# Kernel optimization log

Measured on AMD Instinct MI355X. Metric: run time of the kernel, lower is better.

The kernel has to match this reference:

```python
import jax, jax.numpy as jnp
import numpy as np

B, T = 64, 512
V, E, H, L = 100000, 256, 256, 9


def _lstm(x, Wx, Wh, b):
    # x: [B,T,E] -> hs: [B,T,H]; Keras gate order i,f,c,o
    xg = jnp.einsum('bte,eg->btg', x, Wx) + b  # [B,T,4H]
    h0 = jnp.zeros((x.shape[0], Wh.shape[0]), x.dtype)

    def step(carry, xt):
        h, c = carry
        g = xt + h @ Wh
        i, f, gc, o = jnp.split(g, 4, axis=-1)
        c = jax.nn.sigmoid(f) * c + jax.nn.sigmoid(i) * jnp.tanh(gc)
        h = jax.nn.sigmoid(o) * jnp.tanh(c)
        return (h, c), h

    _, hs = jax.lax.scan(step, (h0, h0), jnp.swapaxes(xg, 0, 1))
    return jnp.swapaxes(hs, 0, 1)


def _crf_log_likelihood(logits, tags, seq_len, trans):
    # logits: [B,T,L], tags: [B,T] int, seq_len: [B] int, trans: [L,L]
    Bb, Tt, Ll = logits.shape
    t_idx = jnp.arange(Tt)
    mask = (t_idx[None, :] < seq_len[:, None]).astype(logits.dtype)  # [B,T]
    # gold path score: unary + pairwise transitions
    unary = jnp.take_along_axis(logits, tags[..., None], axis=-1)[..., 0]  # [B,T]
    unary_score = jnp.sum(unary * mask, axis=-1)
    binary = trans[tags[:, :-1], tags[:, 1:]]  # [B,T-1]
    binary_score = jnp.sum(binary * mask[:, 1:], axis=-1)
    score = unary_score + binary_score
    # forward algorithm (log partition)
    alpha0 = logits[:, 0]  # [B,L]
    step_mask = t_idx[1:, None] < seq_len[None, :]  # [T-1,B]

    def step(alpha, xs):
        logit_t, m = xs  # [B,L], [B]
        new = jax.nn.logsumexp(alpha[:, :, None] + trans[None], axis=1) + logit_t
        alpha = jnp.where(m[:, None], new, alpha)
        return alpha, None

    alpha, _ = jax.lax.scan(step, alpha0, (jnp.swapaxes(logits[:, 1:], 0, 1), step_mask))
    log_norm = jax.nn.logsumexp(alpha, axis=-1)  # [B]
    return score - log_norm


def setup_inputs() -> dict:
    key = jax.random.key(0)
    ks = jax.random.split(key, 12)
    s = 0.05
    return {
        'tokens': jax.random.randint(ks[0], (B, T), 0, V),
        'labels': jax.random.randint(ks[1], (B, T), 0, L),
        'emb_table': jax.random.normal(ks[2], (V, E), jnp.float32) * s,
        'Wx_f': jax.random.normal(ks[3], (E, 4 * H), jnp.float32) * s,
        'Wh_f': jax.random.normal(ks[4], (H, 4 * H), jnp.float32) * s,
        'b_f': jnp.zeros((4 * H,), jnp.float32),
        'Wx_b': jax.random.normal(ks[5], (E, 4 * H), jnp.float32) * s,
        'Wh_b': jax.random.normal(ks[6], (H, 4 * H), jnp.float32) * s,
        'b_b': jnp.zeros((4 * H,), jnp.float32),
        'W_dense': jax.random.normal(ks[7], (2 * H, L), jnp.float32) * s,
        'b_dense': jnp.zeros((L,), jnp.float32),
        'trans': jax.random.uniform(ks[8], (L, L), jnp.float32),
    }


def reference(tokens, labels, emb_table, Wx_f, Wh_f, b_f, Wx_b, Wh_b, b_b, W_dense, b_dense, trans):
    # seq_len = count of non-pad (nonzero) tokens, as in the original call()
    seq_len = jnp.sum((tokens != 0).astype(jnp.int32), axis=-1)  # [B]
    emb = emb_table[tokens]  # [B,T,E]  (dropout inactive at inference)
    h_fwd = _lstm(emb, Wx_f, Wh_f, b_f)
    h_bwd = _lstm(emb[:, ::-1], Wx_b, Wh_b, b_b)[:, ::-1]
    enc = jnp.concatenate([h_fwd, h_bwd], axis=-1)  # [B,T,2H]
    logits = enc @ W_dense + b_dense  # [B,T,L]
    ll = _crf_log_likelihood(logits, labels, seq_len, trans)  # [B]
    return logits, seq_len, ll
```

## Files before the change

### kernel.cpp

```cpp
#include <hip/hip_runtime.h>
#include <hip/hip_fp16.h>


typedef unsigned int  uint32;
typedef unsigned short ushort16;
typedef __attribute__((ext_vector_type(8))) short  short8;
typedef __attribute__((ext_vector_type(4))) float  floatx4;
typedef __attribute__((ext_vector_type(2))) _Float16 half2t;

#define BB 64
#define TT 512
#define NT (BB*TT)
#define G4 1024
#define NL 9
#define KR 92
#define KL 36

__device__ inline float bf2f(ushort16 u) {
  return __builtin_bit_cast(float, ((uint32)u) << 16);
}
__device__ inline ushort16 f2bf(float f) {
  uint32 u = __builtin_bit_cast(uint32, f);
  u += 0x7fffu + ((u >> 16) & 1u);
  return (ushort16)(u >> 16);
}
__device__ inline float sigf(float x)  { return 1.0f / (1.0f + __expf(-x)); }
__device__ inline float tanhf_(float x){ return 1.0f - 2.0f / (1.0f + __expf(2.0f * x)); }

__device__ inline float fdot2_(uint32 w, half2t h, float acc) {
  return __builtin_amdgcn_fdot2(__builtin_bit_cast(half2t, w), h, acc, false);
}

__global__ __launch_bounds__(64) void k_seqlen(const int* __restrict__ tokens,
                                               int* __restrict__ slen,
                                               float* __restrict__ out_sl) {
  const int b = blockIdx.x, lane = threadIdx.x;
  int cnt = 0;
  for (int t = lane; t < TT; t += 64) cnt += (tokens[b * TT + t] != 0) ? 1 : 0;
  #pragma unroll
  for (int off = 32; off >= 1; off >>= 1) cnt += __shfl_down(cnt, off, 64);
  if (lane == 0) { slen[b] = cnt; out_sl[b] = (float)cnt; }
}

__global__ __launch_bounds__(256) void k_embed(const int* __restrict__ tokens,
                                               const float* __restrict__ emb,
                                               ushort16* __restrict__ A) {
  const int f = blockIdx.x * 256 + threadIdx.x;
  const int e = f * 4;
  const int row = e >> 8;
  const int col = e & 255;
  const int tok = tokens[row];
  const float4 v = *(const float4*)(emb + (size_t)tok * 256 + col);
  uint32 lo = (uint32)f2bf(v.x) | ((uint32)f2bf(v.y) << 16);
  uint32 hi = (uint32)f2bf(v.z) | ((uint32)f2bf(v.w) << 16);
  *(uint2*)(A + e) = make_uint2(lo, hi);
}

__global__ __launch_bounds__(256) void k_wxprep(const float* __restrict__ Wxf,
                                                const float* __restrict__ Wxb,
                                                ushort16* __restrict__ BT) {
  const int id = blockIdx.x * 256 + threadIdx.x;
  const int c = id >> 8, k = id & 255;
  const float v = (c < G4) ? Wxf[k * G4 + c] : Wxb[k * G4 + (c - G4)];
  BT[c * 256 + k] = f2bf(v);
}

__global__ __launch_bounds__(256) void k_whprep(const float* __restrict__ Wh,
                                                uint32* __restrict__ W2) {
  const int id = blockIdx.x * 256 + threadIdx.x;
  const int k2 = id >> 10, c = id & 1023;
  const float w0 = Wh[(2 * k2) * G4 + c];
  const float w1 = Wh[(2 * k2 + 1) * G4 + c];
  const ushort16 b0 = __builtin_bit_cast(ushort16, (_Float16)w0);
  const ushort16 b1 = __builtin_bit_cast(ushort16, (_Float16)w1);
  W2[id] = ((uint32)b1 << 16) | (uint32)b0;
}

__global__ __launch_bounds__(256) void k_gemm_xg(const ushort16* __restrict__ A,
                                                 const ushort16* __restrict__ BT,
                                                 const float* __restrict__ bias_f,
                                                 const float* __restrict__ bias_b,
                                                 ushort16* __restrict__ xgf,
                                                 ushort16* __restrict__ xgb) {
  __shared__ __align__(16) ushort16 As[64 * 36];
  __shared__ __align__(16) ushort16 Bs[64 * 36];
  const int m0 = blockIdx.x * 64;
  const int n0 = blockIdx.y * 64;
  const int tid = threadIdx.x;
  const int wave = tid >> 6, lane = tid & 63;
  const int lr = tid >> 2;
  const int lc = (tid & 3) * 8;
  const int am = lane & 15, aq = lane >> 4;
  floatx4 acc[4];
  #pragma unroll
  for (int j = 0; j < 4; ++j) acc[j] = (floatx4){0.f, 0.f, 0.f, 0.f};

  for (int k0 = 0; k0 < 256; k0 += 32) {
    const uint4 va = *(const uint4*)(A  + ((m0 + lr) * 256 + k0 + lc));
    const uint4 vb = *(const uint4*)(BT + ((n0 + lr) * 256 + k0 + lc));
    *(uint2*)&As[lr * 36 + lc]     = make_uint2(va.x, va.y);
    *(uint2*)&As[lr * 36 + lc + 4] = make_uint2(va.z, va.w);
    *(uint2*)&Bs[lr * 36 + lc]     = make_uint2(vb.x, vb.y);
    *(uint2*)&Bs[lr * 36 + lc + 4] = make_uint2(vb.z, vb.w);
    __syncthreads();
    union { uint2 u[2]; short8 s; } fa, fb;
    fa.u[0] = *(const uint2*)&As[(wave * 16 + am) * 36 + aq * 8];
    fa.u[1] = *(const uint2*)&As[(wave * 16 + am) * 36 + aq * 8 + 4];
    #pragma unroll
    for (int j = 0; j < 4; ++j) {
      fb.u[0] = *(const uint2*)&Bs[(j * 16 + am) * 36 + aq * 8];
      fb.u[1] = *(const uint2*)&Bs[(j * 16 + am) * 36 + aq * 8 + 4];
      acc[j] = __builtin_amdgcn_mfma_f32_16x16x32_bf16(fa.s, fb.s, acc[j], 0, 0, 0);
    }
    __syncthreads();
  }
  const int orow = m0 + wave * 16 + aq * 4;
  #pragma unroll
  for (int j = 0; j < 4; ++j) {
    const int col = n0 + j * 16 + am;
    const float bv = (col < G4) ? bias_f[col] : bias_b[col - G4];
    #pragma unroll
    for (int r = 0; r < 4; ++r) {
      const float v = acc[j][r] + bv;
      const int row = orow + r;
      if (col < G4) xgf[row * G4 + col] = f2bf(v);
      else          xgb[row * G4 + (col - G4)] = f2bf(v);
    }
  }
}

__global__ __launch_bounds__(512, 2) void k_lstm(const ushort16* __restrict__ xgf,
                                                 const ushort16* __restrict__ xgb,
                                                 const uint32* __restrict__ Whf,
                                                 const uint32* __restrict__ Whb,
                                                 float* __restrict__ enc) {
  __shared__ uint32 WL[KL * 1024];
  __shared__ float gate[1024];
  __shared__ __align__(16) uint32 h2buf[2][128];
  const int bi = blockIdx.x;
  const int dir = bi >> 6, b = bi & 63;
  const int tid = threadIdx.x;
  const int w = tid >> 6, l = tid & 63;
  const int colA = w * 128 + l;
  const int colB = colA + 64;
  const ushort16* xg = dir ? xgb : xgf;
  const uint32* W2 = dir ? Whb : Whf;

  for (int idx = tid; idx < KL * 1024; idx += 512) {
    const int k2r = idx >> 10, c = idx & 1023;
    WL[(c >> 7) * (KL * 128) + k2r * 128 + ((c & 63) << 1) + ((c >> 6) & 1)] =
        W2[(KR + k2r) * 1024 + c];
  }
  uint32 wA[KR], wB[KR];
  #pragma unroll
  for (int i = 0; i < KR; ++i) {
    wA[i] = W2[i * 1024 + colA];
    wB[i] = W2[i * 1024 + colB];
  }
  #pragma unroll
  for (int i = 0; i < KR; ++i) asm volatile("" : "+v"(wA[i]), "+v"(wB[i]));

  if (tid < 128) h2buf[0][tid] = 0u;
  float c_state = 0.f;
  __syncthreads();

  const uint32* wl = WL + w * (KL * 128) + (l << 1);
  {
  }
  const int t0 = dir ? (TT - 1) : 0;
  ushort16 xA = xg[(size_t)(b * TT + t0) * G4 + colA];
  ushort16 xB = xg[(size_t)(b * TT + t0) * G4 + colB];

  for (int s = 0; s < TT; ++s) {
    float acc0 = bf2f(xA);
    float acc1 = 0.f;
    float acc2 = bf2f(xB);
    float acc3 = 0.f;
    if (s + 1 < TT) {
      const int t1 = dir ? (TT - 2 - s) : (s + 1);
      const ushort16* xr1 = xg + (size_t)(b * TT + t1) * G4;
      xA = xr1[colA];
      xB = xr1[colB];
    }
    const uint4* hb = (const uint4*)h2buf[s & 1];
    #pragma unroll
    for (int blk = 0; blk < 32; ++blk) {
      const uint4 hq = hb[blk];
      #pragma unroll
      for (int j = 0; j < 4; ++j) {
        const int k2 = blk * 4 + j;
        const uint32 hu = (j == 0) ? hq.x : (j == 1) ? hq.y : (j == 2) ? hq.z : hq.w;
        const half2t hh = __builtin_bit_cast(half2t, hu);
        if (k2 < KR) {
          if (j & 1) { acc1 = fdot2_(wA[k2], hh, acc1); acc3 = fdot2_(wB[k2], hh, acc3); }
          else       { acc0 = fdot2_(wA[k2], hh, acc0); acc2 = fdot2_(wB[k2], hh, acc2); }
        } else {
          const uint2 wp = *(const uint2*)(wl + (k2 - KR) * 128);
          if (j & 1) { acc1 = fdot2_(wp.x, hh, acc1); acc3 = fdot2_(wp.y, hh, acc3); }
          else       { acc0 = fdot2_(wp.x, hh, acc0); acc2 = fdot2_(wp.y, hh, acc2); }
        }
      }
    }
    gate[colA] = acc0 + acc1;
    gate[colB] = acc2 + acc3;
    __syncthreads();
    if (tid < 256) {
      const float gi = gate[tid];
      const float gf = gate[256 + tid];
      const float gg = gate[512 + tid];
      const float go = gate[768 + tid];
      c_state = sigf(gf) * c_state + sigf(gi) * tanhf_(gg);
      const float h = sigf(go) * tanhf_(c_state);
      const int row = b * TT + (dir ? (TT - 1 - s) : s);
      enc[(size_t)row * 512 + dir * 256 + tid] = h;
      const int hv = (int)(uint32)__builtin_bit_cast(ushort16, (_Float16)h);
      const int ho = __shfl_xor(hv, 1, 64);
      if (!(tid & 1))
        h2buf[(s + 1) & 1][tid >> 1] = ((uint32)hv & 0xffffu) | ((uint32)ho << 16);
    }
    __syncthreads();
  }
}

__global__ __launch_bounds__(256) void k_dense(const float* __restrict__ enc,
                                               const float* __restrict__ Wd,
                                               const float* __restrict__ bd,
                                               float* __restrict__ logits) {
  __shared__ float Wl[512 * NL];
  __shared__ float bl[NL];
  const int tid = threadIdx.x;
  for (int i = tid; i < 512 * NL; i += 256) Wl[i] = Wd[i];
  if (tid < NL) bl[tid] = bd[tid];
  __syncthreads();
  const int wave = tid >> 6, lane = tid & 63;
  const int row = blockIdx.x * 4 + wave;
  const float* er = enc + (size_t)row * 512;
  float p[NL];
  #pragma unroll
  for (int c = 0; c < NL; ++c) p[c] = 0.f;
  #pragma unroll
  for (int u = 0; u < 8; ++u) {
    const int k = u * 64 + lane;
    const float v = er[k];
    const float* wr = &Wl[k * NL];
    #pragma unroll
    for (int c = 0; c < NL; ++c) p[c] += v * wr[c];
  }
  #pragma unroll
  for (int c = 0; c < NL; ++c) {
    #pragma unroll
    for (int off = 32; off >= 1; off >>= 1) p[c] += __shfl_down(p[c], off, 64);
  }
  if (lane == 0) {
    float* orow = logits + (size_t)row * NL;
    #pragma unroll
    for (int c = 0; c < NL; ++c) orow[c] = p[c] + bl[c];
  }
}

__global__ __launch_bounds__(64) void k_crf(const float* __restrict__ logits,
                                            const int* __restrict__ labels,
                                            const int* __restrict__ slen,
                                            const float* __restrict__ trans,
                                            float* __restrict__ out_ll) {
  __shared__ float tr[NL * NL];
  __shared__ float alpha[NL];
  const int b = blockIdx.x;
  const int lane = threadIdx.x;
  for (int i = lane; i < NL * NL; i += 64) tr[i] = trans[i];
  __syncthreads();
  const int len = slen[b];
  const int* tg = labels + b * TT;
  const float* lg = logits + (size_t)b * TT * NL;
  float s = 0.f;
  for (int t = lane; t < TT; t += 64)
    if (t < len) s += lg[t * NL + tg[t]];
  for (int t = lane; t < TT - 1; t += 64)
    if (t + 1 < len) s += tr[tg[t] * NL + tg[t + 1]];
  #pragma unroll
  for (int off = 32; off >= 1; off >>= 1) s += __shfl_down(s, off, 64);
  if (lane < NL) alpha[lane] = lg[lane];
  __syncthreads();
  if (lane < NL) {
    const int j = lane;
    for (int t = 1; t < TT; ++t) {
      if (t < len) {
        float av[NL];
        float m = -1e30f;
        #pragma unroll
        for (int i = 0; i < NL; ++i) { av[i] = alpha[i] + tr[i * NL + j]; m = fmaxf(m, av[i]); }
        float ss = 0.f;
        #pragma unroll
        for (int i = 0; i < NL; ++i) ss += __expf(av[i] - m);
        const float nj = m + __logf(ss) + lg[t * NL + j];
        alpha[j] = nj;
      }
    }
  }
  __syncthreads();
  if (lane == 0) {
    float m = -1e30f;
    #pragma unroll
    for (int i = 0; i < NL; ++i) m = fmaxf(m, alpha[i]);
    float ss = 0.f;
    #pragma unroll
    for (int i = 0; i < NL; ++i) ss += __expf(alpha[i] - m);
    out_ll[b] = s - (m + __logf(ss));
  }
}

extern "C" void kernel_launch(void* const* d_in, const int* in_sizes, int n_in,
                              void* d_out, int out_size, void* d_ws, size_t ws_size,
                              hipStream_t stream) {
  (void)in_sizes; (void)n_in; (void)out_size; (void)ws_size;
  const int*   tokens = (const int*)d_in[0];
  const int*   labels = (const int*)d_in[1];
  const float* emb    = (const float*)d_in[2];
  const float* Wxf    = (const float*)d_in[3];
  const float* Whf    = (const float*)d_in[4];
  const float* bf_    = (const float*)d_in[5];
  const float* Wxb    = (const float*)d_in[6];
  const float* Whb    = (const float*)d_in[7];
  const float* bb_    = (const float*)d_in[8];
  const float* Wd     = (const float*)d_in[9];
  const float* bd     = (const float*)d_in[10];
  const float* trans  = (const float*)d_in[11];
  float* out = (float*)d_out;

  char* ws = (char*)d_ws;
  ushort16* A    = (ushort16*)(ws + 0);
  ushort16* BT   = (ushort16*)(ws + 16777216);
  uint32*   W2f  = (uint32*)  (ws + 17825792);
  uint32*   W2b  = (uint32*)  (ws + 18350080);
  ushort16* xgf  = (ushort16*)(ws + 18874368);
  ushort16* xgb  = (ushort16*)(ws + 85983232);
  float*    enc  = (float*)   (ws + 153092096);
  int*      slen = (int*)     (ws + 220200960);

  k_seqlen<<<BB, 64, 0, stream>>>(tokens, slen, out + NT * NL);
  k_embed <<<NT * 256 / 4 / 256, 256, 0, stream>>>(tokens, emb, A);
  k_wxprep<<<2048 * 256 / 256, 256, 0, stream>>>(Wxf, Wxb, BT);
  k_whprep<<<128 * 1024 / 256, 256, 0, stream>>>(Whf, W2f);
  k_whprep<<<128 * 1024 / 256, 256, 0, stream>>>(Whb, W2b);
  k_gemm_xg<<<dim3(NT / 64, 2048 / 64), 256, 0, stream>>>(A, BT, bf_, bb_, xgf, xgb);
  k_lstm  <<<128, 512, 0, stream>>>(xgf, xgb, W2f, W2b, enc);
  k_dense <<<NT / 4, 256, 0, stream>>>(enc, Wd, bd, out);
  k_crf   <<<BB, 64, 0, stream>>>(out, labels, slen, trans, out + NT * NL + BB);
}
```

Before: 1.403 ms.

## Keep LSTM recurrent weights in AGPRs and pack xg gate pairs per thread

The recurrent-weight register arrays in the LSTM kernel now live in accumulator registers (AGPRs), written once with v_accvgpr_write and read back each step with v_accvgpr_read. This frees architectural VGPRs so more weights can stay in registers rather than spill. Separately, the xg GEMM epilogue writes its output in a permuted layout so each LSTM thread fetches its two gate inputs with one 32-bit load instead of two 16-bit loads. The cost is an extra accvgpr read per weight on every timestep of the serial recurrence.

Result: slower. 1.919 ms (+36.8%).

```diff
diff --git a/kernel.cpp b/kernel.cpp
--- a/kernel.cpp
+++ b/kernel.cpp
@@ -119,18 +119,20 @@
   for (int j = 0; j < 4; ++j) {
     const int col = n0 + j * 16 + am;
     const float bv = (col < G4) ? bias_f[col] : bias_b[col - G4];
+    const int cc = col & 1023;
+    const int poff = ((cc >> 7) * 64 + (cc & 63)) * 2 + ((cc >> 6) & 1);
+    ushort16* dst = (col < G4) ? xgf : xgb;
     #pragma unroll
     for (int r = 0; r < 4; ++r) {
       const float v = acc[j][r] + bv;
       const int row = orow + r;
-      if (col < G4) xgf[row * G4 + col] = f2bf(v);
-      else          xgb[row * G4 + (col - G4)] = f2bf(v);
-    }
-  }
-}
-
-__global__ __launch_bounds__(512, 2) void k_lstm(const ushort16* __restrict__ xgf,
-                                                 const ushort16* __restrict__ xgb,
+      dst[(size_t)row * G4 + poff] = f2bf(v);
+    }
+  }
+}
+
+__global__ __launch_bounds__(512, 2) void k_lstm(const uint32* __restrict__ xgf,
+                                                 const uint32* __restrict__ xgb,
                                                  const uint32* __restrict__ Whf,
                                                  const uint32* __restrict__ Whb,
                                                  float* __restrict__ enc) {
@@ -143,7 +145,7 @@
   const int w = tid >> 6, l = tid & 63;
   const int colA = w * 128 + l;
   const int colB = colA + 64;
-  const ushort16* xg = dir ? xgb : xgf;
+  const uint32* xg = dir ? xgb : xgf;
   const uint32* W2 = dir ? Whb : Whf;
 
   for (int idx = tid; idx < KL * 1024; idx += 512) {
@@ -151,36 +153,31 @@
     WL[(c >> 7) * (KL * 128) + k2r * 128 + ((c & 63) << 1) + ((c >> 6) & 1)] =
         W2[(KR + k2r) * 1024 + c];
   }
-  uint32 wA[KR], wB[KR];
+  uint32 awA[KR], awB[KR];
   #pragma unroll
   for (int i = 0; i < KR; ++i) {
-    wA[i] = W2[i * 1024 + colA];
-    wB[i] = W2[i * 1024 + colB];
-  }
-  #pragma unroll
-  for (int i = 0; i < KR; ++i) asm volatile("" : "+v"(wA[i]), "+v"(wB[i]));
+    const uint32 va = W2[i * 1024 + colA];
+    const uint32 vb = W2[i * 1024 + colB];
+    asm volatile("v_accvgpr_write_b32 %0, %1" : "=a"(awA[i]) : "v"(va));
+    asm volatile("v_accvgpr_write_b32 %0, %1" : "=a"(awB[i]) : "v"(vb));
+  }
 
   if (tid < 128) h2buf[0][tid] = 0u;
   float c_state = 0.f;
   __syncthreads();
 
   const uint32* wl = WL + w * (KL * 128) + (l << 1);
-  {
-  }
   const int t0 = dir ? (TT - 1) : 0;
-  ushort16 xA = xg[(size_t)(b * TT + t0) * G4 + colA];
-  ushort16 xB = xg[(size_t)(b * TT + t0) * G4 + colB];
+  uint32 xpair = xg[(size_t)(b * TT + t0) * 512 + w * 64 + l];
 
   for (int s = 0; s < TT; ++s) {
-    float acc0 = bf2f(xA);
+    float acc0 = bf2f((ushort16)(xpair & 0xffffu));
     float acc1 = 0.f;
-    float acc2 = bf2f(xB);
+    float acc2 = bf2f((ushort16)(xpair >> 16));
     float acc3 = 0.f;
     if (s + 1 < TT) {
       const int t1 = dir ? (TT - 2 - s) : (s + 1);
-      const ushort16* xr1 = xg + (size_t)(b * TT + t1) * G4;
-      xA = xr1[colA];
-      xB = xr1[colB];
+      xpair = xg[(size_t)(b * TT + t1) * 512 + w * 64 + l];
     }
     const uint4* hb = (const uint4*)h2buf[s & 1];
     #pragma unroll
@@ -192,8 +189,11 @@
         const uint32 hu = (j == 0) ? hq.x : (j == 1) ? hq.y : (j == 2) ? hq.z : hq.w;
         const half2t hh = __builtin_bit_cast(half2t, hu);
         if (k2 < KR) {
-          if (j & 1) { acc1 = fdot2_(wA[k2], hh, acc1); acc3 = fdot2_(wB[k2], hh, acc3); }
-          else       { acc0 = fdot2_(wA[k2], hh, acc0); acc2 = fdot2_(wB[k2], hh, acc2); }
+          uint32 wa, wb;
+          asm volatile("v_accvgpr_read_b32 %0, %1" : "=v"(wa) : "a"(awA[k2]));
+          asm volatile("v_accvgpr_read_b32 %0, %1" : "=v"(wb) : "a"(awB[k2]));
+          if (j & 1) { acc1 = fdot2_(wa, hh, acc1); acc3 = fdot2_(wb, hh, acc3); }
+          else       { acc0 = fdot2_(wa, hh, acc0); acc2 = fdot2_(wb, hh, acc2); }
         } else {
           const uint2 wp = *(const uint2*)(wl + (k2 - KR) * 128);
           if (j & 1) { acc1 = fdot2_(wp.x, hh, acc1); acc3 = fdot2_(wp.y, hh, acc3); }
@@ -343,7 +343,7 @@
   k_whprep<<<128 * 1024 / 256, 256, 0, stream>>>(Whf, W2f);
   k_whprep<<<128 * 1024 / 256, 256, 0, stream>>>(Whb, W2b);
   k_gemm_xg<<<dim3(NT / 64, 2048 / 64), 256, 0, stream>>>(A, BT, bf_, bb_, xgf, xgb);
-  k_lstm  <<<128, 512, 0, stream>>>(xgf, xgb, W2f, W2b, enc);
+  k_lstm  <<<128, 512, 0, stream>>>((const uint32*)xgf, (const uint32*)xgb, W2f, W2b, enc);
   k_dense <<<NT / 4, 256, 0, stream>>>(enc, Wd, bd, out);
   k_crf   <<<BB, 64, 0, stream>>>(out, labels, slen, trans, out + NT * NL + BB);
 }
```
